# Optimization experiments

Measured on AMD Instinct MI355X. Metric: run time of the kernel, lower is better.

Reference implementation:

```python
import jax, jax.numpy as jnp
import numpy as np

N_FEATURES = 256  # channels; vectors have sizes 2..256 (255 vectors)
EPS = 1e-16


def _pad_mask(m, n):
    # row i holds a vector of size i+2, right-aligned; left part is constant 1-padding
    return jnp.arange(n)[None, :] >= (n - 2 - jnp.arange(m))[:, None]


def setup_inputs() -> dict:
    key = jax.random.key(0)
    k1, k2, k3 = jax.random.split(key, 3)
    B, C, H, W = 32, N_FEATURES, 64, 64
    x = jax.random.normal(k1, (B, C, H, W), dtype=jnp.float32)
    log_det_jac = jnp.zeros((B,), dtype=jnp.float32)
    z = jax.random.normal(k2, (B, 16), dtype=jnp.float32)
    V = jax.random.normal(k3, (C - 1, C), dtype=jnp.float32)
    # mimic reset_parameters: each vector scaled to unit norm (over its real entries)
    mask = _pad_mask(C - 1, C)
    norms = jnp.sqrt(jnp.sum(jnp.where(mask, V, 0.0) ** 2, axis=1, keepdims=True)) + EPS
    V = V / norms
    return {"x": x, "log_det_jac": log_det_jac, "z": z, "V": V}


def _cascade(V, n):
    # Q <- Q @ (I - 2 v v^T / (v.v + eps)) applied sequentially == rank-1 update
    mask = _pad_mask(V.shape[0], n)
    Vfull = jnp.where(mask, V, 1.0)  # prepend ones like householder_matrix

    def step(Q, v):
        inner = jnp.dot(v, v) + EPS
        Qv = Q @ v  # [n]
        return Q - (2.0 / inner) * jnp.outer(Qv, v), None

    Q0 = jnp.eye(n, dtype=V.dtype)
    Q, _ = jax.lax.scan(step, Q0, Vfull)
    return Q


def reference(x, log_det_jac, z, V):
    W = _cascade(V, N_FEATURES)  # [C, C] orthogonal
    # 1x1 conv: y[b,o,h,w] = sum_c W[o,c] x[b,c,h,w]
    y = jnp.einsum('oc,bchw->bohw', W, x)
    return y, log_det_jac + 0.0, z
```

## Files before the change

kernel.cpp:

```cpp
#include <hip/hip_runtime.h>
#include <stdint.h>

typedef __attribute__((ext_vector_type(8))) short short8v;
typedef __attribute__((ext_vector_type(4))) float f32x4;

__device__ __forceinline__ unsigned short f2bf(float f) {
  union { float f; unsigned int i; } v; v.f = f;
  unsigned int x = v.i;
  x += 0x7FFFu + ((x >> 16) & 1u);
  return (unsigned short)(x >> 16);
}

__global__ void __launch_bounds__(256) prep_kernel(const float* __restrict__ V,
                                                   float* __restrict__ Vs) {
  const int k = blockIdx.x;
  const int c = threadIdx.x;
  float val = (c >= 254 - k) ? V[k * 256 + c] : 1.0f;
  float ss = val * val;
  #pragma unroll
  for (int off = 32; off >= 1; off >>= 1) ss += __shfl_xor(ss, off);
  __shared__ float part[4];
  if ((threadIdx.x & 63) == 0) part[threadIdx.x >> 6] = ss;
  __syncthreads();
  const float tot = part[0] + part[1] + part[2] + part[3];
  const float s = sqrtf(2.0f / (tot + 1e-16f));
  Vs[k * 256 + c] = s * val;
}

__global__ void __launch_bounds__(256) cascade_kernel(const float* __restrict__ Vs,
                                                      unsigned short* __restrict__ Wb) {
  const int w = threadIdx.x >> 6;
  const int l = threadIdx.x & 63;
  const int r0 = blockIdx.x * 16 + w * 4;

  f32x4 q[4];
  #pragma unroll
  for (int j = 0; j < 4; ++j) {
    const int r = r0 + j;
    q[j][0] = (4 * l + 0 == r) ? 1.0f : 0.0f;
    q[j][1] = (4 * l + 1 == r) ? 1.0f : 0.0f;
    q[j][2] = (4 * l + 2 == r) ? 1.0f : 0.0f;
    q[j][3] = (4 * l + 3 == r) ? 1.0f : 0.0f;
  }

  const f32x4* __restrict__ Vs4 = (const f32x4*)Vs;
  f32x4 vn = Vs4[l];
  for (int k = 0; k < 255; ++k) {
    const f32x4 v = vn;
    if (k + 1 < 255) vn = Vs4[(k + 1) * 64 + l];
    float p[4];
    #pragma unroll
    for (int j = 0; j < 4; ++j)
      p[j] = q[j][0] * v[0] + q[j][1] * v[1] + q[j][2] * v[2] + q[j][3] * v[3];
    #pragma unroll
    for (int off = 32; off >= 1; off >>= 1) {
      #pragma unroll
      for (int j = 0; j < 4; ++j) p[j] += __shfl_xor(p[j], off);
    }
    #pragma unroll
    for (int j = 0; j < 4; ++j) {
      q[j][0] -= p[j] * v[0];
      q[j][1] -= p[j] * v[1];
      q[j][2] -= p[j] * v[2];
      q[j][3] -= p[j] * v[3];
    }
  }

  #pragma unroll
  for (int j = 0; j < 4; ++j) {
    ushort4 o;
    o.x = f2bf(q[j][0]); o.y = f2bf(q[j][1]); o.z = f2bf(q[j][2]); o.w = f2bf(q[j][3]);
    *(ushort4*)(Wb + (size_t)(r0 + j) * 256 + 4 * l) = o;
  }
}

__global__ void __launch_bounds__(256) conv_kernel(const float* __restrict__ x,
                                                   const unsigned short* __restrict__ Wb,
                                                   float* __restrict__ y) {
  const int b  = blockIdx.y;
  const int n0 = blockIdx.x * 64;
  const int w  = threadIdx.x >> 6;
  const int l  = threadIdx.x & 63;
  const int lr = l & 15;
  const int lg = l >> 4;

  const float* __restrict__ xb = x + (size_t)b * (256u * 4096u);
  float* __restrict__ yb = y + (size_t)b * (256u * 4096u);

  f32x4 acc[4][4];
  #pragma unroll
  for (int i = 0; i < 4; ++i)
    #pragma unroll
    for (int j = 0; j < 4; ++j)
      acc[i][j] = (f32x4){0.f, 0.f, 0.f, 0.f};

  for (int k0 = 0; k0 < 256; k0 += 32) {
    short8v a[4];
    #pragma unroll
    for (int i = 0; i < 4; ++i)
      a[i] = *(const short8v*)(Wb + (size_t)(64 * w + 16 * i + lr) * 256 + k0 + 8 * lg);

    short8v bb[4];
    #pragma unroll
    for (int jn = 0; jn < 4; ++jn) {
      const float* __restrict__ bp =
          xb + (size_t)(k0 + 8 * lg) * 4096 + n0 + 16 * jn + lr;
      short8v t;
      #pragma unroll
      for (int j = 0; j < 8; ++j) t[j] = (short)f2bf(bp[(size_t)j * 4096]);
      bb[jn] = t;
    }

    #pragma unroll
    for (int i = 0; i < 4; ++i)
      #pragma unroll
      for (int jn = 0; jn < 4; ++jn)
        acc[i][jn] = __builtin_amdgcn_mfma_f32_16x16x32_bf16(a[i], bb[jn], acc[i][jn], 0, 0, 0);
  }

  #pragma unroll
  for (int i = 0; i < 4; ++i)
    #pragma unroll
    for (int jn = 0; jn < 4; ++jn)
      #pragma unroll
      for (int rr = 0; rr < 4; ++rr) {
        const int o = 64 * w + 16 * i + 4 * lg + rr;
        yb[(size_t)o * 4096 + n0 + 16 * jn + lr] = acc[i][jn][rr];
      }
}

__global__ void tail_kernel(const float* __restrict__ ldj,
                            const float* __restrict__ z,
                            float* __restrict__ out) {
  const int t = threadIdx.x;
  if (t < 32)  out[33554432u + t] = ldj[t];
  if (t < 512) out[33554464u + t] = z[t];
}

extern "C" void kernel_launch(void* const* d_in, const int* in_sizes, int n_in,
                              void* d_out, int out_size, void* d_ws, size_t ws_size,
                              hipStream_t stream) {
  const float* x   = (const float*)d_in[0];
  const float* ldj = (const float*)d_in[1];
  const float* z   = (const float*)d_in[2];
  const float* V   = (const float*)d_in[3];
  float* out = (float*)d_out;

  float* Vs = (float*)d_ws;
  unsigned short* Wb = (unsigned short*)((char*)d_ws + 1048576);

  prep_kernel<<<255, 256, 0, stream>>>(V, Vs);
  cascade_kernel<<<16, 256, 0, stream>>>(Vs, Wb);
  dim3 grid(64, 32);
  conv_kernel<<<grid, 256, 0, stream>>>(x, Wb, out);
  tail_kernel<<<1, 512, 0, stream>>>(ldj, z, out);
}
```

Baseline: 162.6 us.

## Stage x tiles through swizzled LDS with coalesced float4 loads and fold tail into prep

The conv kernel now loads x with coalesced float4 reads, converts the values to bf16 pairs, and stages them in a swizzled shared-memory tile. The next k-chunk is prefetched into registers while the current one feeds MFMA. Blocks grow to 512 threads, each wave taking 32 output rows, which halves the accumulators per wave. The separate tail kernel is removed and its copies of ldj and z are done by an extra block in prep_kernel, saving one launch. The cost is added __syncthreads barriers and shared-memory traffic in each k-step.

```diff
diff --git a/kernel.cpp b/kernel.cpp
--- a/kernel.cpp
+++ b/kernel.cpp
@@ -12,9 +12,18 @@
 }
 
 __global__ void __launch_bounds__(256) prep_kernel(const float* __restrict__ V,
-                                                   float* __restrict__ Vs) {
+                                                   float* __restrict__ Vs,
+                                                   const float* __restrict__ ldj,
+                                                   const float* __restrict__ z,
+                                                   float* __restrict__ out) {
   const int k = blockIdx.x;
   const int c = threadIdx.x;
+  if (k == 255) {
+    if (c < 32) out[33554432u + c] = ldj[c];
+    out[33554464u + c] = z[c];
+    out[33554464u + 256u + c] = z[256u + c];
+    return;
+  }
   float val = (c >= 254 - k) ? V[k * 256 + c] : 1.0f;
   float ss = val * val;
   #pragma unroll
@@ -74,67 +83,90 @@
   }
 }
 
-__global__ void __launch_bounds__(256) conv_kernel(const float* __restrict__ x,
+__global__ void __launch_bounds__(512) conv_kernel(const float* __restrict__ x,
                                                    const unsigned short* __restrict__ Wb,
                                                    float* __restrict__ y) {
+  __shared__ unsigned int lds[2048];
+
   const int b  = blockIdx.y;
   const int n0 = blockIdx.x * 64;
-  const int w  = threadIdx.x >> 6;
-  const int l  = threadIdx.x & 63;
+  const int t  = threadIdx.x;
+  const int w  = t >> 6;
+  const int l  = t & 63;
   const int lr = l & 15;
   const int lg = l >> 4;
+  const int nq = t & 15;
+  const int kb = t >> 4;
 
   const float* __restrict__ xb = x + (size_t)b * (256u * 4096u);
   float* __restrict__ yb = y + (size_t)b * (256u * 4096u);
 
-  f32x4 acc[4][4];
+  f32x4 acc[2][4];
   #pragma unroll
-  for (int i = 0; i < 4; ++i)
+  for (int i = 0; i < 2; ++i)
     #pragma unroll
     for (int j = 0; j < 4; ++j)
       acc[i][j] = (f32x4){0.f, 0.f, 0.f, 0.f};
 
-  for (int k0 = 0; k0 < 256; k0 += 32) {
-    short8v a[4];
+  f32x4 r0, r1;
+  {
+    const f32x4* p = (const f32x4*)(xb + (size_t)(2 * kb) * 4096 + n0) + nq;
+    r0 = p[0];
+    r1 = p[1024];
+  }
+
+  for (int T = 0; T < 4; ++T) {
+    unsigned int packed[4];
     #pragma unroll
-    for (int i = 0; i < 4; ++i)
-      a[i] = *(const short8v*)(Wb + (size_t)(64 * w + 16 * i + lr) * 256 + k0 + 8 * lg);
+    for (int j = 0; j < 4; ++j)
+      packed[j] = (unsigned int)f2bf(r0[j]) | ((unsigned int)f2bf(r1[j]) << 16);
 
-    short8v bb[4];
+    if (T) __syncthreads();
     #pragma unroll
-    for (int jn = 0; jn < 4; ++jn) {
-      const float* __restrict__ bp =
-          xb + (size_t)(k0 + 8 * lg) * 4096 + n0 + 16 * jn + lr;
-      short8v t;
-      #pragma unroll
-      for (int j = 0; j < 8; ++j) t[j] = (short)f2bf(bp[(size_t)j * 4096]);
-      bb[jn] = t;
+    for (int jj = 0; jj < 4; ++jj) {
+      const int j = (jj + nq) & 3;
+      const int n = 4 * nq + j;
+      const int dw = n * 32 + ((((kb >> 2) ^ (n & 7)) << 2) | (kb & 3));
+      lds[dw] = packed[j];
+    }
+    __syncthreads();
+
+    if (T < 3) {
+      const f32x4* p = (const f32x4*)(xb + (size_t)(64 * (T + 1) + 2 * kb) * 4096 + n0) + nq;
+      r0 = p[0];
+      r1 = p[1024];
     }
 
     #pragma unroll
-    for (int i = 0; i < 4; ++i)
+    for (int s = 0; s < 2; ++s) {
+      short8v a[2], bb[4];
       #pragma unroll
-      for (int jn = 0; jn < 4; ++jn)
-        acc[i][jn] = __builtin_amdgcn_mfma_f32_16x16x32_bf16(a[i], bb[jn], acc[i][jn], 0, 0, 0);
+      for (int i = 0; i < 2; ++i)
+        a[i] = *(const short8v*)(Wb + (size_t)(32 * w + 16 * i + lr) * 256
+                                 + 64 * T + 32 * s + 8 * lg);
+      #pragma unroll
+      for (int jn = 0; jn < 4; ++jn) {
+        const int n = 16 * jn + lr;
+        const int dw = n * 32 + ((((s << 2) + lg) ^ (lr & 7)) << 2);
+        bb[jn] = *(const short8v*)(&lds[dw]);
+      }
+      #pragma unroll
+      for (int i = 0; i < 2; ++i)
+        #pragma unroll
+        for (int jn = 0; jn < 4; ++jn)
+          acc[i][jn] = __builtin_amdgcn_mfma_f32_16x16x32_bf16(a[i], bb[jn], acc[i][jn], 0, 0, 0);
+    }
   }
 
   #pragma unroll
-  for (int i = 0; i < 4; ++i)
+  for (int i = 0; i < 2; ++i)
     #pragma unroll
     for (int jn = 0; jn < 4; ++jn)
       #pragma unroll
       for (int rr = 0; rr < 4; ++rr) {
-        const int o = 64 * w + 16 * i + 4 * lg + rr;
+        const int o = 32 * w + 16 * i + 4 * lg + rr;
         yb[(size_t)o * 4096 + n0 + 16 * jn + lr] = acc[i][jn][rr];
       }
-}
-
-__global__ void tail_kernel(const float* __restrict__ ldj,
-                            const float* __restrict__ z,
-                            float* __restrict__ out) {
-  const int t = threadIdx.x;
-  if (t < 32)  out[33554432u + t] = ldj[t];
-  if (t < 512) out[33554464u + t] = z[t];
 }
 
 extern "C" void kernel_launch(void* const* d_in, const int* in_sizes, int n_in,
@@ -149,9 +181,8 @@
   float* Vs = (float*)d_ws;
   unsigned short* Wb = (unsigned short*)((char*)d_ws + 1048576);
 
-  prep_kernel<<<255, 256, 0, stream>>>(V, Vs);
+  prep_kernel<<<256, 256, 0, stream>>>(V, Vs, ldj, z, out);
   cascade_kernel<<<16, 256, 0, stream>>>(Vs, Wb);
   dim3 grid(64, 32);
-  conv_kernel<<<grid, 256, 0, stream>>>(x, Wb, out);
-  tail_kernel<<<1, 512, 0, stream>>>(ldj, z, out);
+  conv_kernel<<<grid, 512, 0, stream>>>(x, Wb, out);
 }
```

After: 154.1 us. 1.06x faster.
